# Optimization experiments

Hardware: AMD Instinct MI355X
Metric: run time of the kernel (lower is better)

The kernel has to match this reference:

```python
import jax, jax.numpy as jnp
import numpy as np

N = 100000
E = 1600000
IN_DIM = 256
HID = 128


def setup_inputs() -> dict:
    key = jax.random.key(0)
    k = jax.random.split(key, 8)
    x = jax.random.normal(k[0], (N, IN_DIM), dtype=jnp.float32)
    edge_index = jax.random.randint(k[1], (2, E), 0, N, dtype=jnp.int64 if jax.config.jax_enable_x64 else jnp.int32)
    # GCNConv weight (no bias pre-aggregation; bias added after aggregation, as in PyG)
    W_conv = jax.random.normal(k[2], (IN_DIM, HID), dtype=jnp.float32) / np.sqrt(IN_DIM)
    b_conv = jnp.zeros((HID,), dtype=jnp.float32)
    prelu_a = jnp.full((1,), 0.25, dtype=jnp.float32)  # torch.nn.PReLU default init
    W_lin = jax.random.normal(k[3], (HID, IN_DIM), dtype=jnp.float32) / np.sqrt(HID)
    b_lin = jnp.zeros((IN_DIM,), dtype=jnp.float32)
    return {"x": x, "edge_index": edge_index, "W_conv": W_conv, "b_conv": b_conv,
            "prelu_a": prelu_a, "W_lin": W_lin, "b_lin": b_lin}


def _gcn_conv(x, edge_index, W, b):
    # h = x @ W  ([N, HID])
    h = x @ W
    src, dst = edge_index[0], edge_index[1]
    # add self-loops
    loops = jnp.arange(N, dtype=src.dtype)
    src = jnp.concatenate([src, loops])
    dst = jnp.concatenate([dst, loops])
    # symmetric degree normalization deg^-1/2 (degree over incoming edges incl. self-loops)
    deg = jax.ops.segment_sum(jnp.ones_like(dst, dtype=h.dtype), dst, num_segments=N)
    dinv = jnp.where(deg > 0, jax.lax.rsqrt(deg), 0.0)
    norm = dinv[src] * dinv[dst]                     # [E+N]
    msg = h[src] * norm[:, None]                     # gather + scale  [E+N, HID]
    out = jax.ops.segment_sum(msg, dst, num_segments=N)  # scatter-add  [N, HID]
    return out + b


def reference(x, edge_index, W_conv, b_conv, prelu_a, W_lin, b_lin):
    h = _gcn_conv(x, edge_index, W_conv, b_conv)
    h = jnp.where(h >= 0, h, prelu_a * h)            # PReLU (single shared slope)
    # dropout p=0.0 -> identity
    return h @ W_lin + b_lin                          # [N, IN_DIM]
```

## Files before the change

### kernel.cpp

```cpp
#include <hip/hip_runtime.h>

#define N_NODES 100000
#define E_EDGES 1600000
#define INDIM 256
#define HID 128
#define CAP 64
#define NPART 8
#define PART_SZ 12500
#define ECAP 32768
#define PA_BLOCKS 1563
#define PA_STRIDE (PA_BLOCKS * 256)

typedef __attribute__((ext_vector_type(8))) short s16x8;
typedef __attribute__((ext_vector_type(4))) float f32x4;

__device__ __forceinline__ unsigned short cvt_bf16(float f) {
    unsigned int u = __float_as_uint(f);
    u += 0x7FFFu + ((u >> 16) & 1u);
    return (unsigned short)(u >> 16);
}
__device__ __forceinline__ float bf16_to_f(unsigned short s) {
    return __uint_as_float(((unsigned int)s) << 16);
}

__global__ __launch_bounds__(256) void parta_kernel(const int* __restrict__ src,
                                                    const int* __restrict__ dst,
                                                    int* __restrict__ gcnt,
                                                    unsigned int* __restrict__ pedges) {
    __shared__ int sCount[8];
    __shared__ int sBase[8];
    const int tid = threadIdx.x;
    if (tid < 8) sCount[tid] = 0;
    __syncthreads();
    const int lane = tid & 63;
    const int t0 = blockIdx.x * 256 + tid;
    const int xcd = blockIdx.x & 7;

    unsigned int pk[4];
    int pp[4];
    int lo[4];
#pragma unroll
    for (int r = 0; r < 4; ++r) {
        int e = t0 + r * PA_STRIDE;
        bool valid = e < E_EDGES;
        int d = 0, s = 0;
        if (valid) { d = dst[e]; s = src[e]; }
        int p = valid ? d / PART_SZ : 8;
        unsigned long long mask_p = 0ull;
#pragma unroll
        for (int v = 0; v < 8; ++v) {
            unsigned long long mv = __ballot(p == v);
            if (p == v) mask_p = mv;
        }
        int off = __popcll(mask_p & ((1ull << lane) - 1ull));
        int ldr = (mask_p == 0ull) ? 0 : (__ffsll(mask_p) - 1);
        int wbase = 0;
        if (valid && lane == ldr) wbase = atomicAdd(&sCount[p], __popcll(mask_p));
        wbase = __shfl(wbase, ldr);
        pp[r] = p;
        lo[r] = wbase + off;
        pk[r] = ((unsigned int)(d - p * PART_SZ) << 17) | (unsigned int)s;
    }
    __syncthreads();
    if (tid < 8) sBase[tid] = atomicAdd(&gcnt[xcd * 8 + tid], sCount[tid]);
    __syncthreads();
#pragma unroll
    for (int r = 0; r < 4; ++r) {
        if (pp[r] < 8) {
            int pos = sBase[pp[r]] + lo[r];
            if (pos < ECAP)
                pedges[(size_t)(xcd * 8 + pp[r]) * ECAP + pos] = pk[r];
        }
    }
}

__global__ __launch_bounds__(256) void partb_kernel(const unsigned int* __restrict__ pedges,
                                                    const int* __restrict__ gcnt,
                                                    int* __restrict__ count,
                                                    int* __restrict__ bucket) {
    const int part = blockIdx.x & 7;
    const int bslot = blockIdx.x >> 3;
    const int tid = threadIdx.x;
#pragma unroll
    for (int x = 0; x < 8; ++x) {
        int n = gcnt[x * 8 + part];
        if (n > ECAP) n = ECAP;
        const unsigned int* lst = pedges + (size_t)(x * 8 + part) * ECAP;
        for (int i = bslot * 256 + tid; i < n; i += 128 * 256) {
            unsigned int v = lst[i];
            int s = (int)(v & 0x1FFFFu);
            int d = part * PART_SZ + (int)(v >> 17);
            int slot = atomicAdd(&count[d], 1);
            if (slot < CAP) bucket[d * CAP + slot] = s;
        }
    }
}

__global__ __launch_bounds__(256) void prep_kernel(const float* __restrict__ Wc,
                                                   const float* __restrict__ Wl,
                                                   unsigned short* __restrict__ f1,
                                                   unsigned short* __restrict__ f2) {
    int tid = blockIdx.x * 256 + threadIdx.x;
    if (tid < 32768) {
        int j = tid & 7, L = (tid >> 3) & 63, t = (tid >> 9) & 7, c = tid >> 12;
        int k = c * 32 + ((L >> 4) * 8) + j;
        int n = t * 16 + (L & 15);
        f1[tid] = cvt_bf16(Wc[k * 128 + n]);
    } else {
        int u = tid - 32768;
        int j = u & 7, L = (u >> 3) & 63, t = (u >> 9) & 15, c = u >> 13;
        int k = c * 32 + ((L >> 4) * 8) + j;
        int n = t * 16 + (L & 15);
        f2[u] = cvt_bf16(Wl[k * 256 + n]);
    }
}

__global__ __launch_bounds__(256) void gemm1_kernel(const float* __restrict__ x,
                                                    const unsigned short* __restrict__ fragW,
                                                    unsigned short* __restrict__ h) {
    __shared__ __align__(16) unsigned short xs[64 * 48];
    const int tid = threadIdx.x;
    const int r0 = blockIdx.x * 64;
    const int w = tid >> 6, lane = tid & 63;
    const int q = lane >> 4, m = lane & 15;
    const int srow = tid >> 2, skg = tid & 3;

    f32x4 acc[8];
#pragma unroll
    for (int t = 0; t < 8; ++t) acc[t] = (f32x4){0.f, 0.f, 0.f, 0.f};

    const s16x8* fwv = (const s16x8*)fragW;

    for (int c = 0; c < 8; ++c) {
        int gr = r0 + srow;
        float4 v0 = make_float4(0.f, 0.f, 0.f, 0.f), v1 = v0;
        if (gr < N_NODES) {
            const float* p = &x[(size_t)gr * INDIM + c * 32 + skg * 8];
            v0 = *(const float4*)p;
            v1 = *(const float4*)(p + 4);
        }
        uint4 pk;
        pk.x = ((unsigned)cvt_bf16(v0.y) << 16) | cvt_bf16(v0.x);
        pk.y = ((unsigned)cvt_bf16(v0.w) << 16) | cvt_bf16(v0.z);
        pk.z = ((unsigned)cvt_bf16(v1.y) << 16) | cvt_bf16(v1.x);
        pk.w = ((unsigned)cvt_bf16(v1.w) << 16) | cvt_bf16(v1.z);
        *(uint4*)&xs[srow * 48 + skg * 8] = pk;
        __syncthreads();

        s16x8 a = *(const s16x8*)&xs[(w * 16 + m) * 48 + q * 8];
#pragma unroll
        for (int t = 0; t < 8; ++t) {
            s16x8 b = fwv[(c * 8 + t) * 64 + lane];
            acc[t] = __builtin_amdgcn_mfma_f32_16x16x32_bf16(a, b, acc[t], 0, 0, 0);
        }
        __syncthreads();
    }

    const int row_base = r0 + w * 16 + q * 4;
#pragma unroll
    for (int t = 0; t < 8; ++t) {
#pragma unroll
        for (int r = 0; r < 4; ++r) {
            int row = row_base + r;
            if (row < N_NODES) h[(size_t)row * HID + t * 16 + m] = cvt_bf16(acc[t][r]);
        }
    }
}

__global__ __launch_bounds__(256) void gather_kernel(const int* __restrict__ bucket,
                                                     const int* __restrict__ count,
                                                     const unsigned short* __restrict__ h,
                                                     const float* __restrict__ b_conv,
                                                     const float* __restrict__ prelu_a,
                                                     unsigned short* __restrict__ agg) {
    int wid = (blockIdx.x * 256 + threadIdx.x) >> 6;
    int lane = threadIdx.x & 63;
    if (wid >= N_NODES) return;
    const int g = lane >> 4;
    const int l = lane & 15;
    const int raw = count[wid];
    const float dn = rsqrtf((float)(raw + 1));
    int deg = raw > CAP ? CAP : raw;
    const uint4* hp4 = (const uint4*)h;

    int s_l = wid;
    float dv_l = 0.f;
    if (lane < deg) {
        s_l = bucket[wid * CAP + lane];
        dv_l = rsqrtf((float)(count[s_l] + 1));
    }

    float acc[8];
    {
        uint4 hv = hp4[(size_t)wid * 16 + l];
        float w = (g == 0) ? dn * dn : 0.f;
        const unsigned int* pv = (const unsigned int*)&hv;
#pragma unroll
        for (int k = 0; k < 4; ++k) {
            acc[2 * k]     = w * bf16_to_f((unsigned short)(pv[k] & 0xFFFF));
            acc[2 * k + 1] = w * bf16_to_f((unsigned short)(pv[k] >> 16));
        }
    }

    for (int j = 0; j < deg; j += 4) {
        int e = j + g;
        int s = __shfl(s_l, e);
        float w = __shfl(dv_l, e) * dn;
        uint4 hv = hp4[(size_t)s * 16 + l];
        const unsigned int* pv = (const unsigned int*)&hv;
#pragma unroll
        for (int k = 0; k < 4; ++k) {
            acc[2 * k]     += w * bf16_to_f((unsigned short)(pv[k] & 0xFFFF));
            acc[2 * k + 1] += w * bf16_to_f((unsigned short)(pv[k] >> 16));
        }
    }

#pragma unroll
    for (int k = 0; k < 8; ++k) {
        acc[k] += __shfl_xor(acc[k], 16);
        acc[k] += __shfl_xor(acc[k], 32);
    }

    if (g == 0) {
        float a = prelu_a[0];
        float4 b0 = *(const float4*)&b_conv[l * 8];
        float4 b1 = *(const float4*)&b_conv[l * 8 + 4];
        float bc[8] = {b0.x, b0.y, b0.z, b0.w, b1.x, b1.y, b1.z, b1.w};
        unsigned int o[4];
#pragma unroll
        for (int k = 0; k < 4; ++k) {
            float ox = acc[2 * k] + bc[2 * k];
            float oy = acc[2 * k + 1] + bc[2 * k + 1];
            ox = ox >= 0.f ? ox : a * ox;
            oy = oy >= 0.f ? oy : a * oy;
            o[k] = ((unsigned)cvt_bf16(oy) << 16) | cvt_bf16(ox);
        }
        uint4 ov;
        ov.x = o[0]; ov.y = o[1]; ov.z = o[2]; ov.w = o[3];
        ((uint4*)agg)[(size_t)wid * 16 + l] = ov;
    }
}

__global__ __launch_bounds__(256) void gemm2_kernel(const unsigned short* __restrict__ agg,
                                                    const unsigned short* __restrict__ fragW,
                                                    const float* __restrict__ b_lin,
                                                    float* __restrict__ out) {
    __shared__ __align__(16) unsigned short xs[64 * 48];
    const int tid = threadIdx.x;
    const int r0 = blockIdx.x * 64;
    const int w = tid >> 6, lane = tid & 63;
    const int q = lane >> 4, m = lane & 15;
    const int srow = tid >> 2, skg = tid & 3;

    f32x4 acc[16];
#pragma unroll
    for (int t = 0; t < 16; ++t) acc[t] = (f32x4){0.f, 0.f, 0.f, 0.f};

    const s16x8* fwv = (const s16x8*)fragW;
    const uint4* aggv = (const uint4*)agg;

    for (int c = 0; c < 4; ++c) {
        int gr = r0 + srow;
        uint4 pk = make_uint4(0u, 0u, 0u, 0u);
        if (gr < N_NODES) pk = aggv[(size_t)gr * 16 + c * 4 + skg];
        *(uint4*)&xs[srow * 48 + skg * 8] = pk;
        __syncthreads();

        s16x8 a = *(const s16x8*)&xs[(w * 16 + m) * 48 + q * 8];
#pragma unroll
        for (int t = 0; t < 16; ++t) {
            s16x8 b = fwv[(c * 16 + t) * 64 + lane];
            acc[t] = __builtin_amdgcn_mfma_f32_16x16x32_bf16(a, b, acc[t], 0, 0, 0);
        }
        __syncthreads();
    }

    const int row_base = r0 + w * 16 + q * 4;
#pragma unroll
    for (int t = 0; t < 16; ++t) {
        float bias = b_lin[t * 16 + m];
#pragma unroll
        for (int r = 0; r < 4; ++r) {
            int row = row_base + r;
            if (row < N_NODES) out[(size_t)row * INDIM + t * 16 + m] = acc[t][r] + bias;
        }
    }
}

extern "C" void kernel_launch(void* const* d_in, const int* in_sizes, int n_in,
                              void* d_out, int out_size, void* d_ws, size_t ws_size,
                              hipStream_t stream) {
    const float* x       = (const float*)d_in[0];
    const int*   eidx    = (const int*)d_in[1];
    const float* W_conv  = (const float*)d_in[2];
    const float* b_conv  = (const float*)d_in[3];
    const float* prelu_a = (const float*)d_in[4];
    const float* W_lin   = (const float*)d_in[5];
    const float* b_lin   = (const float*)d_in[6];
    float* out = (float*)d_out;

    const int* src = eidx;
    const int* dst = eidx + E_EDGES;

    char* base = (char*)d_ws;
    int*   bucket = (int*)base;
    unsigned short* agg = (unsigned short*)(base + (size_t)N_NODES * CAP * 4);
    int*   count  = (int*)((char*)agg + (size_t)N_NODES * HID * 2);
    int*   gcnt   = count + 100000;
    unsigned short* fragW1 = (unsigned short*)(count + 100352);
    unsigned short* fragW2 = fragW1 + 32768;
    unsigned int* pedges = (unsigned int*)agg;

    unsigned short* h = (unsigned short*)d_out;

    hipMemsetAsync(count, 0, (size_t)100352 * sizeof(int), stream);

    prep_kernel<<<256, 256, 0, stream>>>(W_conv, W_lin, fragW1, fragW2);

    gemm1_kernel<<<(N_NODES + 63) / 64, 256, 0, stream>>>(x, fragW1, h);

    parta_kernel<<<PA_BLOCKS, 256, 0, stream>>>(src, dst, gcnt, pedges);

    partb_kernel<<<1024, 256, 0, stream>>>(pedges, gcnt, count, bucket);

    gather_kernel<<<(N_NODES * 64) / 256 + 1, 256, 0, stream>>>(
        bucket, count, h, b_conv, prelu_a, agg);

    gemm2_kernel<<<(N_NODES + 63) / 64, 256, 0, stream>>>(agg, fragW2, b_lin, out);
}
```

Before: 410.6 us.

## Merge weight prep into partition pass and co-schedule gemm1 with bucket fill

Weight fragment conversion moves into the edge-partition kernel's first blocks. A combined kernel then runs the first GEMM and the bucket-scatter pass as disjoint block ranges, so the compute-bound GEMM can overlap the atomic-heavy scatter. This cuts two launches. The gather kernel maps blocks partition-major, which matches the XCD-interleaved partition layout and should give better L2 locality. Its edge loop also handles two edges per group per iteration to raise memory-level parallelism, at the cost of more registers.

```diff
diff --git a/kernel.cpp b/kernel.cpp
--- a/kernel.cpp
+++ b/kernel.cpp
@@ -10,6 +10,8 @@
 #define ECAP 32768
 #define PA_BLOCKS 1563
 #define PA_STRIDE (PA_BLOCKS * 256)
+#define G1_BLOCKS 1563
+#define PB_BLOCKS 1024
 
 typedef __attribute__((ext_vector_type(8))) short s16x8;
 typedef __attribute__((ext_vector_type(4))) float f32x4;
@@ -26,10 +28,31 @@
 __global__ __launch_bounds__(256) void parta_kernel(const int* __restrict__ src,
                                                     const int* __restrict__ dst,
                                                     int* __restrict__ gcnt,
-                                                    unsigned int* __restrict__ pedges) {
+                                                    unsigned int* __restrict__ pedges,
+                                                    const float* __restrict__ Wc,
+                                                    const float* __restrict__ Wl,
+                                                    unsigned short* __restrict__ f1,
+                                                    unsigned short* __restrict__ f2) {
     __shared__ int sCount[8];
     __shared__ int sBase[8];
     const int tid = threadIdx.x;
+
+    if (blockIdx.x < 256) {
+        int pt = blockIdx.x * 256 + tid;
+        if (pt < 32768) {
+            int j = pt & 7, L = (pt >> 3) & 63, t = (pt >> 9) & 7, c = pt >> 12;
+            int k = c * 32 + ((L >> 4) * 8) + j;
+            int n = t * 16 + (L & 15);
+            f1[pt] = cvt_bf16(Wc[k * 128 + n]);
+        } else {
+            int u = pt - 32768;
+            int j = u & 7, L = (u >> 3) & 63, t = (u >> 9) & 15, c = u >> 13;
+            int k = c * 32 + ((L >> 4) * 8) + j;
+            int n = t * 16 + (L & 15);
+            f2[u] = cvt_bf16(Wl[k * 256 + n]);
+        }
+    }
+
     if (tid < 8) sCount[tid] = 0;
     __syncthreads();
     const int lane = tid & 63;
@@ -74,95 +97,77 @@
     }
 }
 
-__global__ __launch_bounds__(256) void partb_kernel(const unsigned int* __restrict__ pedges,
-                                                    const int* __restrict__ gcnt,
-                                                    int* __restrict__ count,
-                                                    int* __restrict__ bucket) {
-    const int part = blockIdx.x & 7;
-    const int bslot = blockIdx.x >> 3;
-    const int tid = threadIdx.x;
-#pragma unroll
-    for (int x = 0; x < 8; ++x) {
-        int n = gcnt[x * 8 + part];
-        if (n > ECAP) n = ECAP;
-        const unsigned int* lst = pedges + (size_t)(x * 8 + part) * ECAP;
-        for (int i = bslot * 256 + tid; i < n; i += 128 * 256) {
-            unsigned int v = lst[i];
-            int s = (int)(v & 0x1FFFFu);
-            int d = part * PART_SZ + (int)(v >> 17);
-            int slot = atomicAdd(&count[d], 1);
-            if (slot < CAP) bucket[d * CAP + slot] = s;
-        }
-    }
-}
-
-__global__ __launch_bounds__(256) void prep_kernel(const float* __restrict__ Wc,
-                                                   const float* __restrict__ Wl,
-                                                   unsigned short* __restrict__ f1,
-                                                   unsigned short* __restrict__ f2) {
-    int tid = blockIdx.x * 256 + threadIdx.x;
-    if (tid < 32768) {
-        int j = tid & 7, L = (tid >> 3) & 63, t = (tid >> 9) & 7, c = tid >> 12;
-        int k = c * 32 + ((L >> 4) * 8) + j;
-        int n = t * 16 + (L & 15);
-        f1[tid] = cvt_bf16(Wc[k * 128 + n]);
-    } else {
-        int u = tid - 32768;
-        int j = u & 7, L = (u >> 3) & 63, t = (u >> 9) & 15, c = u >> 13;
-        int k = c * 32 + ((L >> 4) * 8) + j;
-        int n = t * 16 + (L & 15);
-        f2[u] = cvt_bf16(Wl[k * 256 + n]);
-    }
-}
-
-__global__ __launch_bounds__(256) void gemm1_kernel(const float* __restrict__ x,
-                                                    const unsigned short* __restrict__ fragW,
-                                                    unsigned short* __restrict__ h) {
+__global__ __launch_bounds__(256) void fat_kernel(const float* __restrict__ x,
+                                                  const unsigned short* __restrict__ fragW,
+                                                  unsigned short* __restrict__ h,
+                                                  const unsigned int* __restrict__ pedges,
+                                                  const int* __restrict__ gcnt,
+                                                  int* __restrict__ count,
+                                                  int* __restrict__ bucket) {
     __shared__ __align__(16) unsigned short xs[64 * 48];
     const int tid = threadIdx.x;
-    const int r0 = blockIdx.x * 64;
-    const int w = tid >> 6, lane = tid & 63;
-    const int q = lane >> 4, m = lane & 15;
-    const int srow = tid >> 2, skg = tid & 3;
-
-    f32x4 acc[8];
-#pragma unroll
-    for (int t = 0; t < 8; ++t) acc[t] = (f32x4){0.f, 0.f, 0.f, 0.f};
-
-    const s16x8* fwv = (const s16x8*)fragW;
-
-    for (int c = 0; c < 8; ++c) {
-        int gr = r0 + srow;
-        float4 v0 = make_float4(0.f, 0.f, 0.f, 0.f), v1 = v0;
-        if (gr < N_NODES) {
-            const float* p = &x[(size_t)gr * INDIM + c * 32 + skg * 8];
-            v0 = *(const float4*)p;
-            v1 = *(const float4*)(p + 4);
-        }
-        uint4 pk;
-        pk.x = ((unsigned)cvt_bf16(v0.y) << 16) | cvt_bf16(v0.x);
-        pk.y = ((unsigned)cvt_bf16(v0.w) << 16) | cvt_bf16(v0.z);
-        pk.z = ((unsigned)cvt_bf16(v1.y) << 16) | cvt_bf16(v1.x);
-        pk.w = ((unsigned)cvt_bf16(v1.w) << 16) | cvt_bf16(v1.z);
-        *(uint4*)&xs[srow * 48 + skg * 8] = pk;
-        __syncthreads();
-
-        s16x8 a = *(const s16x8*)&xs[(w * 16 + m) * 48 + q * 8];
+
+    if (blockIdx.x < G1_BLOCKS) {
+        const int r0 = blockIdx.x * 64;
+        const int w = tid >> 6, lane = tid & 63;
+        const int q = lane >> 4, m = lane & 15;
+        const int srow = tid >> 2, skg = tid & 3;
+
+        f32x4 acc[8];
+#pragma unroll
+        for (int t = 0; t < 8; ++t) acc[t] = (f32x4){0.f, 0.f, 0.f, 0.f};
+
+        const s16x8* fwv = (const s16x8*)fragW;
+
+        for (int c = 0; c < 8; ++c) {
+            int gr = r0 + srow;
+            float4 v0 = make_float4(0.f, 0.f, 0.f, 0.f), v1 = v0;
+            if (gr < N_NODES) {
+                const float* p = &x[(size_t)gr * INDIM + c * 32 + skg * 8];
+                v0 = *(const float4*)p;
+                v1 = *(const float4*)(p + 4);
+            }
+            uint4 pk;
+            pk.x = ((unsigned)cvt_bf16(v0.y) << 16) | cvt_bf16(v0.x);
+            pk.y = ((unsigned)cvt_bf16(v0.w) << 16) | cvt_bf16(v0.z);
+            pk.z = ((unsigned)cvt_bf16(v1.y) << 16) | cvt_bf16(v1.x);
+            pk.w = ((unsigned)cvt_bf16(v1.w) << 16) | cvt_bf16(v1.z);
+            *(uint4*)&xs[srow * 48 + skg * 8] = pk;
+            __syncthreads();
+
+            s16x8 a = *(const s16x8*)&xs[(w * 16 + m) * 48 + q * 8];
+#pragma unroll
+            for (int t = 0; t < 8; ++t) {
+                s16x8 b = fwv[(c * 8 + t) * 64 + lane];
+                acc[t] = __builtin_amdgcn_mfma_f32_16x16x32_bf16(a, b, acc[t], 0, 0, 0);
+            }
+            __syncthreads();
+        }
+
+        const int row_base = r0 + w * 16 + q * 4;
 #pragma unroll
         for (int t = 0; t < 8; ++t) {
-            s16x8 b = fwv[(c * 8 + t) * 64 + lane];
-            acc[t] = __builtin_amdgcn_mfma_f32_16x16x32_bf16(a, b, acc[t], 0, 0, 0);
-        }
-        __syncthreads();
-    }
-
-    const int row_base = r0 + w * 16 + q * 4;
-#pragma unroll
-    for (int t = 0; t < 8; ++t) {
-#pragma unroll
-        for (int r = 0; r < 4; ++r) {
-            int row = row_base + r;
-            if (row < N_NODES) h[(size_t)row * HID + t * 16 + m] = cvt_bf16(acc[t][r]);
+#pragma unroll
+            for (int r = 0; r < 4; ++r) {
+                int row = row_base + r;
+                if (row < N_NODES) h[(size_t)row * HID + t * 16 + m] = cvt_bf16(acc[t][r]);
+            }
+        }
+    } else {
+        const int part = blockIdx.x & 7;
+        const int bslot = (blockIdx.x - G1_BLOCKS) >> 3;
+#pragma unroll
+        for (int xx = 0; xx < 8; ++xx) {
+            int n = gcnt[xx * 8 + part];
+            if (n > ECAP) n = ECAP;
+            const unsigned int* lst = pedges + (size_t)(xx * 8 + part) * ECAP;
+            for (int i = bslot * 256 + tid; i < n; i += (PB_BLOCKS / 8) * 256) {
+                unsigned int v = lst[i];
+                int s = (int)(v & 0x1FFFFu);
+                int d = part * PART_SZ + (int)(v >> 17);
+                int slot = atomicAdd(&count[d], 1);
+                if (slot < CAP) bucket[d * CAP + slot] = s;
+            }
         }
     }
 }
@@ -173,9 +178,11 @@
                                                      const float* __restrict__ b_conv,
                                                      const float* __restrict__ prelu_a,
                                                      unsigned short* __restrict__ agg) {
-    int wid = (blockIdx.x * 256 + threadIdx.x) >> 6;
-    int lane = threadIdx.x & 63;
-    if (wid >= N_NODES) return;
+    const int part = blockIdx.x & 7;
+    const int bidx = blockIdx.x >> 3;
+    const int wv = threadIdx.x >> 6;
+    const int wid = part * PART_SZ + bidx * 4 + wv;
+    const int lane = threadIdx.x & 63;
     const int g = lane >> 4;
     const int l = lane & 15;
     const int raw = count[wid];
@@ -193,25 +200,35 @@
     float acc[8];
     {
         uint4 hv = hp4[(size_t)wid * 16 + l];
-        float w = (g == 0) ? dn * dn : 0.f;
+        float w0 = (g == 0) ? dn * dn : 0.f;
         const unsigned int* pv = (const unsigned int*)&hv;
 #pragma unroll
         for (int k = 0; k < 4; ++k) {
-            acc[2 * k]     = w * bf16_to_f((unsigned short)(pv[k] & 0xFFFF));
-            acc[2 * k + 1] = w * bf16_to_f((unsigned short)(pv[k] >> 16));
-        }
-    }
-
-    for (int j = 0; j < deg; j += 4) {
-        int e = j + g;
-        int s = __shfl(s_l, e);
-        float w = __shfl(dv_l, e) * dn;
-        uint4 hv = hp4[(size_t)s * 16 + l];
-        const unsigned int* pv = (const unsigned int*)&hv;
+            acc[2 * k]     = w0 * bf16_to_f((unsigned short)(pv[k] & 0xFFFF));
+            acc[2 * k + 1] = w0 * bf16_to_f((unsigned short)(pv[k] >> 16));
+        }
+    }
+
+    for (int j = 0; j < deg; j += 8) {
+        int e0 = j + g;
+        int e1 = j + 4 + g;
+        int s0 = __shfl(s_l, e0);
+        int s1 = __shfl(s_l, e1);
+        float w0 = __shfl(dv_l, e0) * dn;
+        float w1 = __shfl(dv_l, e1) * dn;
+        uint4 hv0 = hp4[(size_t)s0 * 16 + l];
+        uint4 hv1 = hp4[(size_t)s1 * 16 + l];
+        const unsigned int* p0 = (const unsigned int*)&hv0;
+        const unsigned int* p1 = (const unsigned int*)&hv1;
 #pragma unroll
         for (int k = 0; k < 4; ++k) {
-            acc[2 * k]     += w * bf16_to_f((unsigned short)(pv[k] & 0xFFFF));
-            acc[2 * k + 1] += w * bf16_to_f((unsigned short)(pv[k] >> 16));
+            acc[2 * k]     += w0 * bf16_to_f((unsigned short)(p0[k] & 0xFFFF));
+            acc[2 * k + 1] += w0 * bf16_to_f((unsigned short)(p0[k] >> 16));
+        }
+#pragma unroll
+        for (int k = 0; k < 4; ++k) {
+            acc[2 * k]     += w1 * bf16_to_f((unsigned short)(p1[k] & 0xFFFF));
+            acc[2 * k + 1] += w1 * bf16_to_f((unsigned short)(p1[k] >> 16));
         }
     }
 
@@ -315,15 +332,13 @@
 
     hipMemsetAsync(count, 0, (size_t)100352 * sizeof(int), stream);
 
-    prep_kernel<<<256, 256, 0, stream>>>(W_conv, W_lin, fragW1, fragW2);
-
-    gemm1_kernel<<<(N_NODES + 63) / 64, 256, 0, stream>>>(x, fragW1, h);
-
-    parta_kernel<<<PA_BLOCKS, 256, 0, stream>>>(src, dst, gcnt, pedges);
-
-    partb_kernel<<<1024, 256, 0, stream>>>(pedges, gcnt, count, bucket);
-
-    gather_kernel<<<(N_NODES * 64) / 256 + 1, 256, 0, stream>>>(
+    parta_kernel<<<PA_BLOCKS, 256, 0, stream>>>(src, dst, gcnt, pedges,
+                                                W_conv, W_lin, fragW1, fragW2);
+
+    fat_kernel<<<G1_BLOCKS + PB_BLOCKS, 256, 0, stream>>>(x, fragW1, h,
+                                                          pedges, gcnt, count, bucket);
+
+    gather_kernel<<<NPART * (PART_SZ / 4), 256, 0, stream>>>(
         bucket, count, h, b_conv, prelu_a, agg);
 
     gemm2_kernel<<<(N_NODES + 63) / 64, 256, 0, stream>>>(agg, fragW2, b_lin, out);
```

New measurement: 389.1 us. 1.06x faster.
